# Kernel tuning notes

Measured on AMD Instinct MI355X. Metric: run time of the kernel, lower is better.

## Reference

```python
import jax, jax.numpy as jnp
import numpy as np

B, C, F_, T = 32, 2, 1024, 512
CF = C * F_
H = 128  # lstm hidden / embedding dim


def setup_inputs() -> dict:
    key = jax.random.key(0)
    ks = jax.random.split(key, 12)
    s = 0.05
    return {
        "x": jax.random.normal(ks[0], (B, C, F_, T), dtype=jnp.float32),
        "W_fc1": jax.random.normal(ks[1], (H, CF), dtype=jnp.float32) * s,
        "b_fc1": jax.random.normal(ks[2], (H,), dtype=jnp.float32) * s,
        "Wih_f": jax.random.normal(ks[3], (4 * H, H), dtype=jnp.float32) * s,
        "Whh_f": jax.random.normal(ks[4], (4 * H, H), dtype=jnp.float32) * s,
        "b_f": jax.random.normal(ks[5], (4 * H,), dtype=jnp.float32) * s,
        "Wih_b": jax.random.normal(ks[6], (4 * H, H), dtype=jnp.float32) * s,
        "Whh_b": jax.random.normal(ks[7], (4 * H, H), dtype=jnp.float32) * s,
        "b_b": jax.random.normal(ks[8], (4 * H,), dtype=jnp.float32) * s,
        "W_out": jax.random.normal(ks[9], (H, 2 * H), dtype=jnp.float32) * s,
        "b_out": jax.random.normal(ks[10], (H,), dtype=jnp.float32) * s,
    }


def _lstm_scan(x, Wih, Whh, b):
    # x: (L, T, H); recurrence over L (torch treats the (B,128) input as an
    # unbatched sequence of length B), vectorized over the T frames.
    L, Tn, _ = x.shape
    Hn = Whh.shape[1]

    def step(carry, xt):
        h, c = carry  # (T, H)
        z = xt @ Wih.T + h @ Whh.T + b  # (T, 4H)
        i, f, g, o = jnp.split(z, 4, axis=-1)
        c = jax.nn.sigmoid(f) * c + jax.nn.sigmoid(i) * jnp.tanh(g)
        h = jax.nn.sigmoid(o) * jnp.tanh(c)
        return (h, c), h

    init = (jnp.zeros((Tn, Hn), x.dtype), jnp.zeros((Tn, Hn), x.dtype))
    _, hs = jax.lax.scan(step, init, x)
    return hs  # (L, T, H)


def reference(x, W_fc1, b_fc1, Wih_f, Whh_f, b_f, Wih_b, Whh_b, b_b, W_out, b_out):
    Bn, Cn, Fn, Tn = x.shape
    # fc1 applied per time frame: (B, CF, T) -> (B, T, 128)
    xr = x.reshape(Bn, Cn * Fn, Tn).transpose(0, 2, 1)
    h = jnp.einsum("btc,dc->btd", xr, W_fc1) + b_fc1
    # bidirectional LSTM over the batch axis (torch unbatched-input semantics)
    hf = _lstm_scan(h, Wih_f, Whh_f, b_f)
    hb = _lstm_scan(h[::-1], Wih_b, Whh_b, b_b)[::-1]
    hs = jnp.concatenate([hf, hb], axis=-1)  # (B, T, 256)
    out = jnp.einsum("btd,ed->bte", hs, W_out) + b_out  # (B, T, 128)
    return out.transpose(0, 2, 1)  # (B, 128, T), matching torch.stack(dim=2)
```

## Files before the change

### kernel.cpp

```cpp
#include <hip/hip_runtime.h>
#include <stdint.h>

typedef __attribute__((ext_vector_type(8))) short short8;
typedef __attribute__((ext_vector_type(4))) float floatx4;

__device__ __forceinline__ float bf16_to_f(uint16_t u) {
    union { uint32_t i; float f; } v; v.i = ((uint32_t)u) << 16; return v.f;
}
__device__ __forceinline__ uint16_t f_to_bf16(float f) {
    union { uint32_t i; float f; } v; v.f = f;
    uint32_t u = v.i;
    u += 0x7FFFu + ((u >> 16) & 1u);
    return (uint16_t)(u >> 16);
}
__device__ __forceinline__ void gload16(const void* g, void* l) {
    __builtin_amdgcn_global_load_lds(
        (const __attribute__((address_space(1))) void*)g,
        (__attribute__((address_space(3))) void*)l, 16, 0, 0);
}
__device__ __forceinline__ float rcpf(float x) { return __builtin_amdgcn_rcpf(x); }

#define B_  32
#define T_  512
#define CF_ 2048
#define H_  128
#define G4_ 512
#define LOG2E 1.4426950408889634f

__global__ __launch_bounds__(256) void k_cvt_all(
        const float* __restrict__ Wfc, const float* __restrict__ Wih_f,
        const float* __restrict__ Wih_b, const float* __restrict__ Whh_f,
        const float* __restrict__ Whh_b, const float* __restrict__ Wout,
        uint16_t* __restrict__ WfcB, uint16_t* __restrict__ WihB,
        uint16_t* __restrict__ WhhB, uint16_t* __restrict__ WoutB) {
    const int blk = blockIdx.x;
    const float* s; uint16_t* d; int off;
    if (blk < 256)      { s = Wfc;   d = WfcB;          off = blk; }
    else if (blk < 320) { s = Wih_f; d = WihB;          off = blk - 256; }
    else if (blk < 384) { s = Wih_b; d = WihB + 65536;  off = blk - 320; }
    else if (blk < 448) { s = Whh_f; d = WhhB;          off = blk - 384; }
    else if (blk < 512) { s = Whh_b; d = WhhB + 65536;  off = blk - 448; }
    else                { s = Wout;  d = WoutB;         off = blk - 512; }
    const int i = off * 1024 + threadIdx.x * 4;
    float4 v = *(const float4*)&s[i];
    ushort4 o;
    o.x = f_to_bf16(v.x); o.y = f_to_bf16(v.y);
    o.z = f_to_bf16(v.z); o.w = f_to_bf16(v.w);
    *(ushort4*)&d[i] = o;
}

__global__ __launch_bounds__(512) void k_fc1x(const float* __restrict__ x,
                                              const uint16_t* __restrict__ WfcB,
                                              const float* __restrict__ bfc,
                                              const uint16_t* __restrict__ WihB,
                                              const float* __restrict__ b_f,
                                              const float* __restrict__ b_b,
                                              uint16_t* __restrict__ Xp) {
    __shared__ float tile[64 * 65];
    __shared__ __align__(16) uint16_t As[8192];
    __shared__ __align__(16) uint16_t Bs[4224];
    __shared__ __align__(16) uint16_t Hs2[8432];

    const int bb = blockIdx.y, n0 = blockIdx.x * 64;
    const int tid = threadIdx.x, w = tid >> 6, l = tid & 63;
    const int lm = l & 15, lk = l >> 4;
    const float* xb = x + (size_t)bb * CF_ * T_;

    const int t4 = (tid & 15) * 4, cf_r = tid >> 4;
    const int kk = (tid & 15) * 4, t_r = tid >> 4;

    float4 xv0, xv1;
    {
        const float* p = &xb[(size_t)(0 + cf_r) * T_ + n0 + t4];
        xv0 = *(const float4*)p;
        xv1 = *(const float4*)(p + 32 * T_);
    }

    const int wmA = (w >> 1) * 32, wnA = (w & 1) * 32;
    floatx4 acc[2][2] = {};
    for (int k0 = 0; k0 < CF_; k0 += 64) {
        __syncthreads();
        tile[(t4 + 0) * 65 + cf_r] = xv0.x;
        tile[(t4 + 1) * 65 + cf_r] = xv0.y;
        tile[(t4 + 2) * 65 + cf_r] = xv0.z;
        tile[(t4 + 3) * 65 + cf_r] = xv0.w;
        tile[(t4 + 0) * 65 + cf_r + 32] = xv1.x;
        tile[(t4 + 1) * 65 + cf_r + 32] = xv1.y;
        tile[(t4 + 2) * 65 + cf_r + 32] = xv1.z;
        tile[(t4 + 3) * 65 + cf_r + 32] = xv1.w;
        gload16(WfcB + (size_t)l * CF_ + k0 + w * 8,        As + (w * 128 + l) * 8);
        gload16(WfcB + (size_t)(64 + l) * CF_ + k0 + w * 8, As + (w * 128 + 64 + l) * 8);
        __syncthreads();
        if (k0 + 64 < CF_) {
            const float* p = &xb[(size_t)(k0 + 64 + cf_r) * T_ + n0 + t4];
            xv0 = *(const float4*)p;
            xv1 = *(const float4*)(p + 32 * T_);
        }
        #pragma unroll
        for (int pass = 0; pass < 2; ++pass) {
            const int tr = t_r + pass * 32;
            ushort4 o;
            o.x = f_to_bf16(tile[tr * 65 + kk + 0]);
            o.y = f_to_bf16(tile[tr * 65 + kk + 1]);
            o.z = f_to_bf16(tile[tr * 65 + kk + 2]);
            o.w = f_to_bf16(tile[tr * 65 + kk + 3]);
            *(ushort4*)&Bs[((kk >> 3) * 66 + tr) * 8 + (kk & 7)] = o;
        }
        __syncthreads();
        short8 a[2][2], bfr[2][2];
        #pragma unroll
        for (int kf = 0; kf < 2; ++kf) {
            #pragma unroll
            for (int mf = 0; mf < 2; ++mf)
                a[mf][kf] = *(const short8*)&As[((kf * 4 + lk) * 128 + wmA + mf * 16 + lm) * 8];
            #pragma unroll
            for (int nf = 0; nf < 2; ++nf)
                bfr[nf][kf] = *(const short8*)&Bs[((kf * 4 + lk) * 66 + wnA + nf * 16 + lm) * 8];
        }
        #pragma unroll
        for (int mf = 0; mf < 2; ++mf)
            #pragma unroll
            for (int nf = 0; nf < 2; ++nf) {
                acc[mf][nf] = __builtin_amdgcn_mfma_f32_16x16x32_bf16(a[mf][0], bfr[nf][0], acc[mf][nf], 0, 0, 0);
                acc[mf][nf] = __builtin_amdgcn_mfma_f32_16x16x32_bf16(a[mf][1], bfr[nf][1], acc[mf][nf], 0, 0, 0);
            }
    }
    __syncthreads();
    #pragma unroll
    for (int mf = 0; mf < 2; ++mf) {
        const int d0 = wmA + mf * 16 + lk * 4;
        const float4 bv = *(const float4*)&bfc[d0];
        const int c = ((wmA + mf * 16) >> 3) + (lk >> 1);
        #pragma unroll
        for (int nf = 0; nf < 2; ++nf) {
            const int t = wnA + nf * 16 + lm;
            ushort4 o;
            o.x = f_to_bf16(acc[mf][nf][0] + bv.x);
            o.y = f_to_bf16(acc[mf][nf][1] + bv.y);
            o.z = f_to_bf16(acc[mf][nf][2] + bv.z);
            o.w = f_to_bf16(acc[mf][nf][3] + bv.w);
            *(ushort4*)&Hs2[(c * 66 + t) * 8 + (lk & 1) * 4] = o;
        }
    }
    __syncthreads();

    const int dirw = w >> 2;
    const int db   = dirw * B_ + bb;
    const uint16_t* Wp = WihB + (size_t)dirw * (G4_ * H_);
    const float* bi = dirw ? b_b : b_f;
    #pragma unroll
    for (int it = 0; it < 2; ++it) {
        const int gbase = (w & 3) * 64 + it * 256;
        short8 aw[4][4];
        #pragma unroll
        for (int mf = 0; mf < 4; ++mf)
            #pragma unroll
            for (int kf = 0; kf < 4; ++kf)
                aw[mf][kf] = *(const short8*)&Wp[(size_t)(gbase + mf * 16 + lm) * H_ + kf * 32 + lk * 8];
        floatx4 acc2[4][4] = {};
        #pragma unroll
        for (int nf = 0; nf < 4; ++nf) {
            short8 bbf[4];
            #pragma unroll
            for (int kf = 0; kf < 4; ++kf)
                bbf[kf] = *(const short8*)&Hs2[((kf * 4 + lk) * 66 + nf * 16 + lm) * 8];
            #pragma unroll
            for (int mf = 0; mf < 4; ++mf)
                #pragma unroll
                for (int kf = 0; kf < 4; ++kf)
                    acc2[mf][nf] = __builtin_amdgcn_mfma_f32_16x16x32_bf16(aw[mf][kf], bbf[kf], acc2[mf][nf], 0, 0, 0);
        }
        #pragma unroll
        for (int mf = 0; mf < 4; ++mf) {
            const int g0 = gbase + mf * 16 + lk * 4;
            const float4 bv = *(const float4*)&bi[g0];
            #pragma unroll
            for (int nf = 0; nf < 4; ++nf) {
                const int t = n0 + nf * 16 + lm;
                ushort4 o;
                o.x = f_to_bf16(acc2[mf][nf][0] + bv.x);
                o.y = f_to_bf16(acc2[mf][nf][1] + bv.y);
                o.z = f_to_bf16(acc2[mf][nf][2] + bv.z);
                o.w = f_to_bf16(acc2[mf][nf][3] + bv.w);
                *(ushort4*)&Xp[((size_t)db * T_ + t) * G4_ + g0] = o;
            }
        }
    }
}

__global__ __launch_bounds__(512) void k_lstm(const uint16_t* __restrict__ Xp,
                                              const uint16_t* __restrict__ WhhB,
                                              uint16_t* __restrict__ hs) {
    __shared__ __align__(16) uint16_t h_sh[16 * 136];
    __shared__ float z_sh[16 * 516];
    const int dir = blockIdx.y, t0 = blockIdx.x * 16;
    const int tid = threadIdx.x, w = tid >> 6, l = tid & 63;
    const int lm = l & 15, lk = l >> 4;
    const int gw = w * 64;
    const uint16_t* Wp = WhhB + dir * (G4_ * H_);

    short8 bw[4][4];
    #pragma unroll
    for (int nf = 0; nf < 4; ++nf)
        #pragma unroll
        for (int kf = 0; kf < 4; ++kf)
            bw[nf][kf] = *(const short8*)&Wp[(size_t)(gw + nf * 16 + lm) * H_ + kf * 32 + lk * 8];

    for (int i = tid; i < 16 * 136; i += 512) h_sh[i] = 0;
    const int hh = tid & 127, tq = tid >> 7;
    float c[4] = {0.f, 0.f, 0.f, 0.f};
    __syncthreads();

    for (int s = 0; s < 32; ++s) {
        const int b_idx = dir ? (31 - s) : s;
        const uint16_t* xp = Xp + ((size_t)(dir * B_ + b_idx) * T_ + t0) * G4_;
        uint16_t xv[4][4];
        #pragma unroll
        for (int j = 0; j < 4; ++j)
            #pragma unroll
            for (int gg = 0; gg < 4; ++gg)
                xv[j][gg] = xp[(size_t)(tq * 4 + j) * G4_ + gg * H_ + hh];

        short8 af[4];
        #pragma unroll
        for (int kf = 0; kf < 4; ++kf)
            af[kf] = *(const short8*)&h_sh[lm * 136 + kf * 32 + lk * 8];
        floatx4 acc[4] = {};
        #pragma unroll
        for (int nf = 0; nf < 4; ++nf)
            #pragma unroll
            for (int kf = 0; kf < 4; ++kf)
                acc[nf] = __builtin_amdgcn_mfma_f32_16x16x32_bf16(af[kf], bw[nf][kf], acc[nf], 0, 0, 0);
        #pragma unroll
        for (int nf = 0; nf < 4; ++nf)
            #pragma unroll
            for (int r = 0; r < 4; ++r)
                z_sh[(lk * 4 + r) * 516 + gw + nf * 16 + lm] = acc[nf][r];
        __syncthreads();

        #pragma unroll
        for (int j = 0; j < 4; ++j) {
            const int t = tq * 4 + j;
            const float* zr = &z_sh[t * 516];
            float zi = zr[hh]            + bf16_to_f(xv[j][0]);
            float zf = zr[H_ + hh]       + bf16_to_f(xv[j][1]);
            float zg = zr[2 * H_ + hh]   + bf16_to_f(xv[j][2]);
            float zo = zr[3 * H_ + hh]   + bf16_to_f(xv[j][3]);
            float si = rcpf(1.f + __builtin_amdgcn_exp2f(-LOG2E * zi));
            float sf = rcpf(1.f + __builtin_amdgcn_exp2f(-LOG2E * zf));
            float so = rcpf(1.f + __builtin_amdgcn_exp2f(-LOG2E * zo));
            float tg = 1.f - 2.f * rcpf(1.f + __builtin_amdgcn_exp2f(2.f * LOG2E * zg));
            c[j] = sf * c[j] + si * tg;
            float tc = 1.f - 2.f * rcpf(1.f + __builtin_amdgcn_exp2f(2.f * LOG2E * c[j]));
            float hn = so * tc;
            uint16_t hb = f_to_bf16(hn);
            h_sh[t * 136 + hh] = hb;
            hs[((size_t)b_idx * T_ + t0 + t) * 256 + dir * H_ + hh] = hb;
        }
        __syncthreads();
    }
}

__global__ __launch_bounds__(256) void k_outm(const uint16_t* __restrict__ WoutB,
                                              const uint16_t* __restrict__ hs,
                                              const float* __restrict__ bout,
                                              float* __restrict__ out) {
    __shared__ __align__(16) uint16_t As[4096], Bs[4096];
    const int b = blockIdx.z, m0 = blockIdx.y * 64, n0 = blockIdx.x * 64;
    const int tid = threadIdx.x, w = tid >> 6, l = tid & 63;
    const int wm = (w >> 1) * 32, wn = (w & 1) * 32;
    const int lm = l & 15, lk = l >> 4;
    const uint16_t* A = WoutB + (size_t)m0 * 256;
    const uint16_t* Bp = hs + ((size_t)b * T_ + n0) * 256;
    floatx4 acc[2][2] = {};
    const uint16_t* gA = A + (size_t)l * 256;
    const uint16_t* gB = Bp + (size_t)l * 256;
    for (int k0 = 0; k0 < 256; k0 += 64) {
        __syncthreads();
        gload16(gA + k0 + (2 * w) * 8,     As + ((2 * w) * 64 + l) * 8);
        gload16(gA + k0 + (2 * w + 1) * 8, As + ((2 * w + 1) * 64 + l) * 8);
        gload16(gB + k0 + (2 * w) * 8,     Bs + ((2 * w) * 64 + l) * 8);
        gload16(gB + k0 + (2 * w + 1) * 8, Bs + ((2 * w + 1) * 64 + l) * 8);
        __syncthreads();
        short8 a[2][2], bfr[2][2];
        #pragma unroll
        for (int kf = 0; kf < 2; ++kf) {
            #pragma unroll
            for (int mf = 0; mf < 2; ++mf)
                a[mf][kf] = *(const short8*)&As[((kf * 4 + lk) * 64 + wm + mf * 16 + lm) * 8];
            #pragma unroll
            for (int nf = 0; nf < 2; ++nf)
                bfr[nf][kf] = *(const short8*)&Bs[((kf * 4 + lk) * 64 + wn + nf * 16 + lm) * 8];
        }
        #pragma unroll
        for (int mf = 0; mf < 2; ++mf)
            #pragma unroll
            for (int nf = 0; nf < 2; ++nf) {
                acc[mf][nf] = __builtin_amdgcn_mfma_f32_16x16x32_bf16(a[mf][0], bfr[nf][0], acc[mf][nf], 0, 0, 0);
                acc[mf][nf] = __builtin_amdgcn_mfma_f32_16x16x32_bf16(a[mf][1], bfr[nf][1], acc[mf][nf], 0, 0, 0);
            }
    }
    #pragma unroll
    for (int mf = 0; mf < 2; ++mf) {
        const int e0 = m0 + wm + mf * 16 + lk * 4;
        const float4 bv = *(const float4*)&bout[e0];
        #pragma unroll
        for (int nf = 0; nf < 2; ++nf) {
            const int t = n0 + wn + nf * 16 + lm;
            out[((size_t)b * H_ + e0 + 0) * T_ + t] = acc[mf][nf][0] + bv.x;
            out[((size_t)b * H_ + e0 + 1) * T_ + t] = acc[mf][nf][1] + bv.y;
            out[((size_t)b * H_ + e0 + 2) * T_ + t] = acc[mf][nf][2] + bv.z;
            out[((size_t)b * H_ + e0 + 3) * T_ + t] = acc[mf][nf][3] + bv.w;
        }
    }
}

extern "C" void kernel_launch(void* const* d_in, const int* in_sizes, int n_in,
                              void* d_out, int out_size, void* d_ws, size_t ws_size,
                              hipStream_t stream) {
    const float* x     = (const float*)d_in[0];
    const float* Wfc   = (const float*)d_in[1];
    const float* bfc   = (const float*)d_in[2];
    const float* Wih_f = (const float*)d_in[3];
    const float* Whh_f = (const float*)d_in[4];
    const float* b_f   = (const float*)d_in[5];
    const float* Wih_b = (const float*)d_in[6];
    const float* Whh_b = (const float*)d_in[7];
    const float* b_b   = (const float*)d_in[8];
    const float* Wout  = (const float*)d_in[9];
    const float* bout  = (const float*)d_in[10];
    float* out = (float*)d_out;

    char* ws = (char*)d_ws;
    uint16_t* Xp    = (uint16_t*)(ws);
    uint16_t* hsB   = (uint16_t*)(ws + 33554432);
    uint16_t* WfcB  = (uint16_t*)(ws + 41943040);
    uint16_t* WihB  = (uint16_t*)(ws + 42467328);
    uint16_t* WhhB  = (uint16_t*)(ws + 42729472);
    uint16_t* WoutB = (uint16_t*)(ws + 42991616);

    k_cvt_all<<<dim3(544), 256, 0, stream>>>(Wfc, Wih_f, Wih_b, Whh_f, Whh_b, Wout,
                                             WfcB, WihB, WhhB, WoutB);
    k_fc1x <<<dim3(8, 32),   512, 0, stream>>>(x, WfcB, bfc, WihB, b_f, b_b, Xp);
    k_lstm <<<dim3(32, 2),   512, 0, stream>>>(Xp, WhhB, hsB);
    k_outm <<<dim3(8, 2, 32), 256, 0, stream>>>(WoutB, hsB, bout, out);
}
```

Measured before the change: 298.7 us.

## Compute LSTM gates in registers, double-buffer hidden state, prefetch next step inputs

Reassigns the gate columns so each lane's MFMA accumulators already hold the i,f,g,o pre-activations for its hidden unit. This removes the z_sh shared-memory round trip and one barrier per timestep. The hidden state is double-buffered in LDS, so only one barrier per step remains, and it uses an LDS-only waitcnt. The next step's input projections are prefetched into registers while the MFMAs run. The cost is more register pressure, and a barrier that does not wait on the in-flight global loads.

```diff
diff --git a/kernel.cpp b/kernel.cpp
--- a/kernel.cpp
+++ b/kernel.cpp
@@ -19,6 +19,12 @@
         (__attribute__((address_space(3))) void*)l, 16, 0, 0);
 }
 __device__ __forceinline__ float rcpf(float x) { return __builtin_amdgcn_rcpf(x); }
+
+__device__ __forceinline__ void bar_lds() {
+    asm volatile("s_waitcnt lgkmcnt(0)" ::: "memory");
+    __builtin_amdgcn_s_barrier();
+    asm volatile("" ::: "memory");
+}
 
 #define B_  32
 #define T_  512
@@ -191,73 +197,80 @@
 __global__ __launch_bounds__(512) void k_lstm(const uint16_t* __restrict__ Xp,
                                               const uint16_t* __restrict__ WhhB,
                                               uint16_t* __restrict__ hs) {
-    __shared__ __align__(16) uint16_t h_sh[16 * 136];
-    __shared__ float z_sh[16 * 516];
+    __shared__ __align__(16) uint16_t h_sh[2][16 * 136];
     const int dir = blockIdx.y, t0 = blockIdx.x * 16;
     const int tid = threadIdx.x, w = tid >> 6, l = tid & 63;
     const int lm = l & 15, lk = l >> 4;
-    const int gw = w * 64;
+    const int gcol = w * 16 + lm;
+    const int tloc = lk * 4;
     const uint16_t* Wp = WhhB + dir * (G4_ * H_);
 
     short8 bw[4][4];
     #pragma unroll
-    for (int nf = 0; nf < 4; ++nf)
+    for (int q = 0; q < 4; ++q)
         #pragma unroll
         for (int kf = 0; kf < 4; ++kf)
-            bw[nf][kf] = *(const short8*)&Wp[(size_t)(gw + nf * 16 + lm) * H_ + kf * 32 + lk * 8];
-
-    for (int i = tid; i < 16 * 136; i += 512) h_sh[i] = 0;
-    const int hh = tid & 127, tq = tid >> 7;
+            bw[q][kf] = *(const short8*)&Wp[(size_t)(q * H_ + gcol) * H_ + kf * 32 + lk * 8];
+
+    for (int i = tid; i < 16 * 136; i += 512) h_sh[0][i] = 0;
     float c[4] = {0.f, 0.f, 0.f, 0.f};
-    __syncthreads();
-
-    for (int s = 0; s < 32; ++s) {
-        const int b_idx = dir ? (31 - s) : s;
-        const uint16_t* xp = Xp + ((size_t)(dir * B_ + b_idx) * T_ + t0) * G4_;
-        uint16_t xv[4][4];
-        #pragma unroll
-        for (int j = 0; j < 4; ++j)
-            #pragma unroll
-            for (int gg = 0; gg < 4; ++gg)
-                xv[j][gg] = xp[(size_t)(tq * 4 + j) * G4_ + gg * H_ + hh];
-
+
+    uint16_t xva[4][4], xvb[4][4];
+    {
+        const int b0 = dir ? (B_ - 1) : 0;
+        const uint16_t* xp = Xp + ((size_t)(dir * B_ + b0) * T_ + t0 + tloc) * G4_;
+        #pragma unroll
+        for (int r = 0; r < 4; ++r)
+            #pragma unroll
+            for (int q = 0; q < 4; ++q)
+                xva[r][q] = xp[(size_t)r * G4_ + q * H_ + gcol];
+    }
+    bar_lds();
+
+    auto step = [&](int s, uint16_t (&xc)[4][4], uint16_t (&xn)[4][4], int par) {
+        const int b_idx = dir ? (B_ - 1 - s) : s;
         short8 af[4];
         #pragma unroll
         for (int kf = 0; kf < 4; ++kf)
-            af[kf] = *(const short8*)&h_sh[lm * 136 + kf * 32 + lk * 8];
+            af[kf] = *(const short8*)&h_sh[par][lm * 136 + kf * 32 + lk * 8];
         floatx4 acc[4] = {};
         #pragma unroll
-        for (int nf = 0; nf < 4; ++nf)
+        for (int q = 0; q < 4; ++q)
             #pragma unroll
             for (int kf = 0; kf < 4; ++kf)
-                acc[nf] = __builtin_amdgcn_mfma_f32_16x16x32_bf16(af[kf], bw[nf][kf], acc[nf], 0, 0, 0);
-        #pragma unroll
-        for (int nf = 0; nf < 4; ++nf)
+                acc[q] = __builtin_amdgcn_mfma_f32_16x16x32_bf16(af[kf], bw[q][kf], acc[q], 0, 0, 0);
+        if (s < B_ - 1) {
+            const int bn = dir ? (B_ - 2 - s) : (s + 1);
+            const uint16_t* xp = Xp + ((size_t)(dir * B_ + bn) * T_ + t0 + tloc) * G4_;
             #pragma unroll
             for (int r = 0; r < 4; ++r)
-                z_sh[(lk * 4 + r) * 516 + gw + nf * 16 + lm] = acc[nf][r];
-        __syncthreads();
-
-        #pragma unroll
-        for (int j = 0; j < 4; ++j) {
-            const int t = tq * 4 + j;
-            const float* zr = &z_sh[t * 516];
-            float zi = zr[hh]            + bf16_to_f(xv[j][0]);
-            float zf = zr[H_ + hh]       + bf16_to_f(xv[j][1]);
-            float zg = zr[2 * H_ + hh]   + bf16_to_f(xv[j][2]);
-            float zo = zr[3 * H_ + hh]   + bf16_to_f(xv[j][3]);
+                #pragma unroll
+                for (int q = 0; q < 4; ++q)
+                    xn[r][q] = xp[(size_t)r * G4_ + q * H_ + gcol];
+        }
+        #pragma unroll
+        for (int r = 0; r < 4; ++r) {
+            float zi = acc[0][r] + bf16_to_f(xc[r][0]);
+            float zf = acc[1][r] + bf16_to_f(xc[r][1]);
+            float zg = acc[2][r] + bf16_to_f(xc[r][2]);
+            float zo = acc[3][r] + bf16_to_f(xc[r][3]);
             float si = rcpf(1.f + __builtin_amdgcn_exp2f(-LOG2E * zi));
             float sf = rcpf(1.f + __builtin_amdgcn_exp2f(-LOG2E * zf));
             float so = rcpf(1.f + __builtin_amdgcn_exp2f(-LOG2E * zo));
             float tg = 1.f - 2.f * rcpf(1.f + __builtin_amdgcn_exp2f(2.f * LOG2E * zg));
-            c[j] = sf * c[j] + si * tg;
-            float tc = 1.f - 2.f * rcpf(1.f + __builtin_amdgcn_exp2f(2.f * LOG2E * c[j]));
+            c[r] = sf * c[r] + si * tg;
+            float tc = 1.f - 2.f * rcpf(1.f + __builtin_amdgcn_exp2f(2.f * LOG2E * c[r]));
             float hn = so * tc;
             uint16_t hb = f_to_bf16(hn);
-            h_sh[t * 136 + hh] = hb;
-            hs[((size_t)b_idx * T_ + t0 + t) * 256 + dir * H_ + hh] = hb;
-        }
-        __syncthreads();
+            h_sh[par ^ 1][(tloc + r) * 136 + gcol] = hb;
+            hs[((size_t)b_idx * T_ + t0 + tloc + r) * 256 + dir * H_ + gcol] = hb;
+        }
+        bar_lds();
+    };
+
+    for (int s2 = 0; s2 < 16; ++s2) {
+        step(2 * s2,     xva, xvb, 0);
+        step(2 * s2 + 1, xvb, xva, 1);
     }
 }
 
```

Result: faster. 278.9 us (median of 2 runs) (-6.6%).
